# Performance work log

Hardware: AMD Instinct MI355X
Metric: run time of the kernel (lower is better)

Reference implementation:

```python
import jax, jax.numpy as jnp
import numpy as np
import math

DIM = 1536
HEAD_DIM = 128
N_HEADS = DIM // HEAD_DIM
B, S = 2, 2048
F, H, W = 8, 16, 16  # F*H*W == S
MAX_POS = 1024
EPS = 1e-6


def _make_freqs():
    # complex rotary freqs per Wan convention, split [22,21,21] over head_dim/2=64
    c = HEAD_DIM // 2
    sizes = [c - 2 * (c // 3), c // 3, c // 3]
    theta = 10000.0
    parts = []
    for s in sizes:
        inv = 1.0 / theta ** (np.arange(s, dtype=np.float64) / s)
        ang = np.arange(MAX_POS, dtype=np.float64)[:, None] * inv[None, :]
        parts.append(np.stack([np.cos(ang), np.sin(ang)], axis=-1))
    return jnp.asarray(np.concatenate(parts, axis=1), dtype=jnp.float32)  # [MAX_POS, 64, 2]


def setup_inputs() -> dict:
    key = jax.random.key(0)
    ks = jax.random.split(key, 12)
    std = 1.0 / math.sqrt(DIM)
    inp = {
        "x": jax.random.normal(ks[0], (B, S, DIM), jnp.float32),
        "seq_lens": jnp.full((B,), S, jnp.int32),
        "grid_sizes": jnp.tile(jnp.array([[F, H, W]], jnp.int32), (B, 1)),
        "freqs": _make_freqs(),
        "Wq": jax.random.normal(ks[1], (DIM, DIM), jnp.float32) * std,
        "bq": jnp.zeros((DIM,), jnp.float32),
        "Wk": jax.random.normal(ks[2], (DIM, DIM), jnp.float32) * std,
        "bk": jnp.zeros((DIM,), jnp.float32),
        "Wv": jax.random.normal(ks[3], (DIM, DIM), jnp.float32) * std,
        "bv": jnp.zeros((DIM,), jnp.float32),
        "Wo": jax.random.normal(ks[4], (DIM, DIM), jnp.float32) * std,
        "bo": jnp.zeros((DIM,), jnp.float32),
        "wq_norm": jnp.ones((DIM,), jnp.float32),
        "wk_norm": jnp.ones((DIM,), jnp.float32),
    }
    return inp


def _rmsnorm(x, w):
    x32 = x.astype(jnp.float32)
    return x32 * jax.lax.rsqrt(jnp.mean(x32 * x32, axis=-1, keepdims=True) + EPS) * w


def _rope_apply(x, grid_sizes, freqs):
    # x: [B, S, N, D]; grid sizes uniform across batch -> vectorized (no per-sample loop)
    f, h, w = (int(v) for v in np.asarray(grid_sizes)[0])
    s_rot = f * h * w
    Bx, Sx, N, D = x.shape
    c = D // 2
    s0, s1 = c - 2 * (c // 3), c // 3
    cos, sin = freqs[..., 0], freqs[..., 1]

    def grid_cs(t):  # build [s_rot, c] table
        tf = jnp.broadcast_to(t[:f, None, None, :s0], (f, h, w, s0))
        th = jnp.broadcast_to(t[None, :h, None, s0:s0 + s1], (f, h, w, s1))
        tw = jnp.broadcast_to(t[None, None, :w, s0 + s1:s0 + 2 * s1], (f, h, w, s1))
        return jnp.concatenate([tf, th, tw], axis=-1).reshape(s_rot, 1, c)

    fc, fs = grid_cs(cos), grid_cs(sin)  # [s_rot, 1, c]
    xr = x[:, :s_rot].astype(jnp.float32).reshape(Bx, s_rot, N, c, 2)
    a, b = xr[..., 0], xr[..., 1]
    out = jnp.stack([a * fc - b * fs, a * fs + b * fc], axis=-1).reshape(Bx, s_rot, N, D)
    if s_rot < Sx:
        out = jnp.concatenate([out, x[:, s_rot:].astype(jnp.float32)], axis=1)
    return out


def reference(x, seq_lens, grid_sizes, freqs, Wq, bq, Wk, bk, Wv, bv, Wo, bo, wq_norm, wk_norm):
    Bx, Sx, dim = x.shape
    N, D = N_HEADS, HEAD_DIM
    q = _rmsnorm(x @ Wq.T + bq, wq_norm).reshape(Bx, Sx, N, D)
    k = _rmsnorm(x @ Wk.T + bk, wk_norm).reshape(Bx, Sx, N, D)
    v = (x @ Wv.T + bv).reshape(Bx, Sx, N, D)
    q = _rope_apply(q, grid_sizes, freqs)
    k = _rope_apply(k, grid_sizes, freqs)
    scores = jnp.einsum("bsnd,btnd->bnst", q, k) / math.sqrt(D)  # [B,N,S,S]
    kmask = jnp.arange(Sx)[None, :] < seq_lens[:, None]          # [B,S] over keys
    scores = jnp.where(kmask[:, None, None, :], scores, -1e30)
    attn = jax.nn.softmax(scores, axis=-1)
    out = jnp.einsum("bnst,btnd->bsnd", attn, v).reshape(Bx, Sx, dim)
    return out @ Wo.T + bo
```

## Files before the change

kernel.cpp:

```cpp
#include <hip/hip_runtime.h>

typedef __attribute__((ext_vector_type(8))) short bf16x8;
typedef __attribute__((ext_vector_type(8))) unsigned short ushort8;
typedef __attribute__((ext_vector_type(4))) float f32x4;
typedef __attribute__((ext_vector_type(16))) float f32x16;
typedef unsigned short u16;
typedef unsigned int u32;

__device__ inline float bf2f(u16 u) {
    unsigned int x = ((unsigned int)u) << 16;
    float f; __builtin_memcpy(&f, &x, 4); return f;
}
__device__ inline u16 f2bf(float f) {
    unsigned int x; __builtin_memcpy(&x, &f, 4);
    unsigned int r = (x + 0x7FFFu + ((x >> 16) & 1u)) >> 16;
    return (u16)r;
}
__device__ inline u32 cvtpk(float lo, float hi) {
    u32 r;
    asm("v_cvt_pk_bf16_f32 %0, %1, %2" : "=v"(r) : "v"(lo), "v"(hi));
    return r;
}
__device__ inline void store_out(u16* p, float v) { *p = f2bf(v); }
__device__ inline void store_out(float* p, float v) { *p = v; }

__global__ __launch_bounds__(256) void f32_to_bf16_kernel(const float* __restrict__ src,
                                                          u16* __restrict__ dst, int n8) {
    int i = blockIdx.x * 256 + threadIdx.x;
    if (i >= n8) return;
    float4 a = *(const float4*)(src + (size_t)i * 8);
    float4 b = *(const float4*)(src + (size_t)i * 8 + 4);
    ushort8 o;
    o[0] = f2bf(a.x); o[1] = f2bf(a.y); o[2] = f2bf(a.z); o[3] = f2bf(a.w);
    o[4] = f2bf(b.x); o[5] = f2bf(b.y); o[6] = f2bf(b.z); o[7] = f2bf(b.w);
    *(ushort8*)(dst + (size_t)i * 8) = o;
}

__global__ __launch_bounds__(256) void prep2_kernel(const float* __restrict__ Wq, const float* __restrict__ Wk,
                                                    const float* __restrict__ Wv, const float* __restrict__ Wo,
                                                    const float* __restrict__ bq, const float* __restrict__ bk,
                                                    const float* __restrict__ bv, const float* __restrict__ freqs,
                                                    u16* __restrict__ wqkv, u16* __restrict__ wob,
                                                    float* __restrict__ bqkv, float* __restrict__ rope) {
    int bid = blockIdx.x, t = threadIdx.x;
    if (bid < 4608) {
        int i = bid * 256 + t;
        int seg = i / 294912, j = i - seg * 294912;
        const float* src = (seg == 0) ? Wq : (seg == 1) ? Wk : (seg == 2) ? Wv : Wo;
        u16* dst = (seg < 3) ? (wqkv + (size_t)seg * 2359296) : wob;
        float4 a = *(const float4*)(src + (size_t)j * 8);
        float4 b = *(const float4*)(src + (size_t)j * 8 + 4);
        ushort8 o;
        o[0] = f2bf(a.x); o[1] = f2bf(a.y); o[2] = f2bf(a.z); o[3] = f2bf(a.w);
        o[4] = f2bf(b.x); o[5] = f2bf(b.y); o[6] = f2bf(b.z); o[7] = f2bf(b.w);
        *(ushort8*)(dst + (size_t)j * 8) = o;
    } else if (bid < 5120) {
        int i = (bid - 4608) * 256 + t;
        int s = i >> 6, j = i & 63;
        int fi = s >> 8, hi = (s >> 4) & 15, wi = s & 15;
        int pos = (j < 22) ? fi : ((j < 43) ? hi : wi);
        rope[s * 128 + j * 2]     = freqs[pos * 128 + j * 2];
        rope[s * 128 + j * 2 + 1] = freqs[pos * 128 + j * 2 + 1];
    } else {
#pragma unroll
        for (int it = 0; it < 18; ++it) {
            int j = it * 256 + t;
            bqkv[j] = (j < 1536) ? bq[j] : ((j < 3072) ? bk[j - 1536] : bv[j - 3072]);
        }
    }
}

template <typename OutT>
__global__ __launch_bounds__(256) void gemm_bt(const u16* __restrict__ A, const u16* __restrict__ Bw,
                                               const float* __restrict__ bias, OutT* __restrict__ C,
                                               int M, int N, int K) {
    __shared__ __align__(16) u16 As[3][4096];
    __shared__ __align__(16) u16 Bs[3][4096];
    const int tid = threadIdx.x;
    const int w = tid >> 6, l = tid & 63;
    const int lg = l >> 4, li = l & 15;
    const int row0 = blockIdx.x * 128, col0 = blockIdx.y * 128;
    const int wr = (w >> 1) * 64, wc = (w & 1) * 64;
    const int nt = K >> 5;

    f32x4 acc[4][4] = {};

    auto STAGE = [&](int bi, int t) {
        int k0 = t << 5;
#pragma unroll
        for (int c = 0; c < 2; ++c) {
            int idx = c * 256 + tid;
            int r = idx >> 2;
            int clog = (idx & 3) ^ ((r >> 1) & 3);
            __builtin_amdgcn_global_load_lds(
                (const __attribute__((address_space(1))) void*)(A + (size_t)(row0 + r) * K + k0 + clog * 8),
                (__attribute__((address_space(3))) void*)((char*)&As[0][0] + bi * 8192 + c * 4096 + w * 1024), 16, 0, 0);
            __builtin_amdgcn_global_load_lds(
                (const __attribute__((address_space(1))) void*)(Bw + (size_t)(col0 + r) * K + k0 + clog * 8),
                (__attribute__((address_space(3))) void*)((char*)&Bs[0][0] + bi * 8192 + c * 4096 + w * 1024), 16, 0, 0);
        }
    };

    const int rchunk = (lg ^ ((li >> 1) & 3)) * 8;
    STAGE(0, 0);
    STAGE(1, 1);
    for (int tb = 0; tb < nt; tb += 3) {
#pragma unroll
        for (int j = 0; j < 3; ++j) {
            const int t = tb + j;
            if (t + 2 < nt) {
                STAGE((j + 2) % 3, t + 2);
                asm volatile("s_waitcnt vmcnt(8)" ::: "memory");
            } else if (t + 1 < nt) {
                asm volatile("s_waitcnt vmcnt(4)" ::: "memory");
            } else {
                asm volatile("s_waitcnt vmcnt(0)" ::: "memory");
            }
            __builtin_amdgcn_s_barrier();
            __builtin_amdgcn_sched_barrier(0);
            const u16* as = &As[j][0];
            const u16* bs = &Bs[j][0];
            bf16x8 af[4], bfr[4];
#pragma unroll
            for (int m = 0; m < 4; ++m) af[m] = *(const bf16x8*)(as + (wr + m * 16 + li) * 32 + rchunk);
#pragma unroll
            for (int n = 0; n < 4; ++n) bfr[n] = *(const bf16x8*)(bs + (wc + n * 16 + li) * 32 + rchunk);
#pragma unroll
            for (int m = 0; m < 4; ++m)
#pragma unroll
                for (int n = 0; n < 4; ++n)
                    acc[m][n] = __builtin_amdgcn_mfma_f32_16x16x32_bf16(af[m], bfr[n], acc[m][n], 0, 0, 0);
            __builtin_amdgcn_sched_barrier(0);
            __builtin_amdgcn_s_barrier();
        }
    }

#pragma unroll
    for (int m = 0; m < 4; ++m) {
#pragma unroll
        for (int n = 0; n < 4; ++n) {
#pragma unroll
            for (int j = 0; j < 4; ++j) {
                int r = row0 + wr + m * 16 + lg * 4 + j;
                int cc = col0 + wc + n * 16 + li;
                float v = acc[m][n][j] + bias[cc];
                store_out(&C[(size_t)r * N + cc], v);
            }
        }
    }
}

__global__ __launch_bounds__(256) void rmsview_kernel(const u16* __restrict__ qkv,
                                                      const float* __restrict__ wq_n,
                                                      const float* __restrict__ wk_n,
                                                      const float* __restrict__ rope,
                                                      u16* __restrict__ qh, u16* __restrict__ kh,
                                                      u16* __restrict__ vt) {
    __shared__ __align__(16) char sm[9216];
    int t = threadIdx.x;
    if (blockIdx.x < 4096) {
        int row = blockIdx.x;
        int b = row >> 11, s = row & 2047;
        const u16* pr = qkv + (size_t)row * 4608;
        int c0 = t * 6;

        float q[6], k[6];
#pragma unroll
        for (int i = 0; i < 3; ++i) {
            ushort2 uq = *(const ushort2*)(pr + c0 + 2 * i);
            ushort2 uk = *(const ushort2*)(pr + 1536 + c0 + 2 * i);
            q[2 * i] = bf2f(uq.x); q[2 * i + 1] = bf2f(uq.y);
            k[2 * i] = bf2f(uk.x); k[2 * i + 1] = bf2f(uk.y);
        }
        float sq = 0.f, sk = 0.f;
#pragma unroll
        for (int i = 0; i < 6; ++i) { sq += q[i] * q[i]; sk += k[i] * k[i]; }
#pragma unroll
        for (int off = 32; off >= 1; off >>= 1) {
            sq += __shfl_down(sq, off);
            sk += __shfl_down(sk, off);
        }
        float* red = (float*)sm;
        int w = t >> 6, l = t & 63;
        if (l == 0) { red[w] = sq; red[w + 4] = sk; }
        __syncthreads();
        float rq = rsqrtf((red[0] + red[1] + red[2] + red[3]) * (1.0f / 1536.0f) + 1e-6f);
        float rk = rsqrtf((red[4] + red[5] + red[6] + red[7]) * (1.0f / 1536.0f) + 1e-6f);

#pragma unroll
        for (int i = 0; i < 3; ++i) {
            int c = c0 + 2 * i;
            int h = c >> 7, d = c & 127;
            float cs = rope[s * 128 + d];
            float sn = rope[s * 128 + d + 1];
            float qa = q[2 * i] * rq * wq_n[c], qb = q[2 * i + 1] * rq * wq_n[c + 1];
            float ka = k[2 * i] * rk * wk_n[c], kb = k[2 * i + 1] * rk * wk_n[c + 1];
            size_t o = ((size_t)(b * 12 + h) * 2048 + s) * 128 + d;
            ushort2 qo, ko;
            qo.x = f2bf(qa * cs - qb * sn); qo.y = f2bf(qa * sn + qb * cs);
            ko.x = f2bf(ka * cs - kb * sn); ko.y = f2bf(ka * sn + kb * cs);
            *(ushort2*)(qh + o) = qo;
            *(ushort2*)(kh + o) = ko;
        }
    } else {
        int idx = blockIdx.x - 4096;
        const int s0 = (idx & 31) * 64;
        const int d0 = ((idx >> 5) & 1) * 64;
        const int bh = idx >> 6;
        const int b = bh / 12, h = bh % 12;
        u16* L = (u16*)sm;

#pragma unroll
        for (int j = 0; j < 2; ++j) {
            int p = j * 256 + t;
            int s = p >> 3, c8 = p & 7;
            ushort8 v8 = *(const ushort8*)(qkv + (size_t)(b * 2048 + s0 + s) * 4608 + 3072 + h * 128 + d0 + c8 * 8);
            int pb = c8 ^ ((s >> 3) & 7);
            *(ushort8*)(L + s * 72 + pb * 8) = v8;
        }
        __syncthreads();
#pragma unroll
        for (int j = 0; j < 2; ++j) {
            int p = j * 256 + t;
            int d = p >> 3, s8 = p & 7;
            ushort8 o;
#pragma unroll
            for (int i = 0; i < 8; ++i) {
                int ps = s8 * 8 + i;
                int v4 = ps & 15;
                int ls = (ps & ~15) | (v4 & 3) | ((v4 & 4) << 1) | ((v4 & 8) >> 1);
                o[i] = L[ls * 72 + ((((d >> 3) ^ (ls >> 3)) & 7) << 3) + (d & 7)];
            }
            *(ushort8*)(vt + (size_t)bh * 128 * 2048 + (size_t)(d0 + d) * 2048 + s0 + s8 * 8) = o;
        }
    }
}

__global__ __launch_bounds__(256, 2) void attn_kernel(const u16* __restrict__ qh, const u16* __restrict__ kh,
                                                      const u16* __restrict__ vt, const int* __restrict__ seq_lens,
                                                      u16* __restrict__ aout) {
    const int bid = blockIdx.x;
    const int g = bid & 7, rr = bid >> 3;
    const int bh = g * 3 + rr % 3;
    const int qt = rr / 3;
    const int b = bh / 12, h = bh % 12;
    const int tid = threadIdx.x;
    const int w = tid >> 6, l = tid & 63;
    const int q5 = l & 31;
    const int hi = l >> 5;
    const int seqlen = seq_lens[b];

    __shared__ __align__(16) char smem[65536];

    const size_t hbase = (size_t)bh * 2048 * 128;
    const u16* kb = kh + hbase;
    const u16* vtb = vt + hbase;

    const int qrow = qt * 128 + w * 32 + q5;
    bf16x8 qf[8];
    {
        const u16* qp = qh + hbase + (size_t)qrow * 128 + hi * 8;
#pragma unroll
        for (int kd = 0; kd < 8; ++kd) qf[kd] = *(const bf16x8*)(qp + kd * 16);
    }

    auto STAGE = [&](int bi, int kv0) {
#pragma unroll
        for (int i = 0; i < 4; ++i) {
            int p = i * 256 + tid;
            int kr = p >> 4, kc = p & 15;
            __builtin_amdgcn_global_load_lds(
                (const __attribute__((address_space(1))) void*)(kb + (size_t)(kv0 + kr) * 128 + ((kc ^ (kr & 15)) << 3)),
                (__attribute__((address_space(3))) void*)(smem + bi * 16384 + i * 4096 + w * 1024), 16, 0, 0);
            int vr = p >> 3, vc = p & 7;
            __builtin_amdgcn_global_load_lds(
                (const __attribute__((address_space(1))) void*)(vtb + (size_t)vr * 2048 + kv0 + ((vc ^ (vr & 7)) << 3)),
                (__attribute__((address_space(3))) void*)(smem + 32768 + bi * 16384 + i * 4096 + w * 1024), 16, 0, 0);
        }
    };

    f32x16 oacc[4] = {};
    float m_run = -3e38f, l_run = 0.f;
    const float c2 = 0.08838834764831845f * 1.44269504088896341f;

    STAGE(0, 0);
    for (int t = 0; t < 32; ++t) {
        const int cur = t & 1;
        const int kv0 = t * 64;
        if (t < 31) {
            STAGE(cur ^ 1, kv0 + 64);
            asm volatile("s_waitcnt vmcnt(8)" ::: "memory");
        } else {
            asm volatile("s_waitcnt vmcnt(0)" ::: "memory");
        }
        __builtin_amdgcn_s_barrier();
        __builtin_amdgcn_sched_barrier(0);

        const u16* Ks = (const u16*)(smem + cur * 16384);
        const u16* Vs = (const u16*)(smem + 32768 + cur * 16384);

        f32x16 sacc[2] = {};
        __builtin_amdgcn_s_setprio(1);
#pragma unroll
        for (int tt = 0; tt < 2; ++tt) {
            int row = tt * 32 + q5;
#pragma unroll
            for (int kd = 0; kd < 8; ++kd) {
                int bk = (2 * kd + hi) ^ (q5 & 15);
                bf16x8 kf = *(const bf16x8*)(Ks + row * 128 + bk * 8);
                sacc[tt] = __builtin_amdgcn_mfma_f32_32x32x16_bf16(kf, qf[kd], sacc[tt], 0, 0, 0);
            }
        }
        __builtin_amdgcn_s_setprio(0);

        if (kv0 + 64 > seqlen) {
#pragma unroll
            for (int tt = 0; tt < 2; ++tt)
#pragma unroll
                for (int m = 0; m < 4; ++m)
#pragma unroll
                    for (int r = 0; r < 4; ++r) {
                        int kv = kv0 + tt * 32 + m * 8 + hi * 4 + r;
                        if (kv >= seqlen) sacc[tt][m * 4 + r] = -1e30f;
                    }
        }

        float a8[8];
#pragma unroll
        for (int r = 0; r < 8; ++r)
            a8[r] = fmaxf(fmaxf(sacc[0][r], sacc[0][r + 8]), fmaxf(sacc[1][r], sacc[1][r + 8]));
        float b4_0 = fmaxf(a8[0], a8[1]), b4_1 = fmaxf(a8[2], a8[3]);
        float b4_2 = fmaxf(a8[4], a8[5]), b4_3 = fmaxf(a8[6], a8[7]);
        float pmax = fmaxf(fmaxf(b4_0, b4_1), fmaxf(b4_2, b4_3));
        pmax = fmaxf(pmax, __shfl_xor(pmax, 32));

        int defer = __all(pmax <= m_run + 62.7f);
        if (!defer) {
            float mnew = fmaxf(m_run, pmax);
            float alpha = __builtin_amdgcn_exp2f((m_run - mnew) * c2);
#pragma unroll
            for (int dt = 0; dt < 4; ++dt)
#pragma unroll
                for (int r = 0; r < 16; ++r) oacc[dt][r] *= alpha;
            l_run *= alpha;
            m_run = mnew;
        }

        float gs[8];
        u32 Wp[2][4][2];
#pragma unroll
        for (int tt = 0; tt < 2; ++tt)
#pragma unroll
            for (int m = 0; m < 4; ++m) {
                float p0 = __builtin_amdgcn_exp2f((sacc[tt][4 * m + 0] - m_run) * c2);
                float p1 = __builtin_amdgcn_exp2f((sacc[tt][4 * m + 1] - m_run) * c2);
                float p2 = __builtin_amdgcn_exp2f((sacc[tt][4 * m + 2] - m_run) * c2);
                float p3 = __builtin_amdgcn_exp2f((sacc[tt][4 * m + 3] - m_run) * c2);
                gs[tt * 4 + m] = (p0 + p1) + (p2 + p3);
                Wp[tt][m][0] = cvtpk(p0, p1);
                Wp[tt][m][1] = cvtpk(p2, p3);
            }
        float ls = ((gs[0] + gs[1]) + (gs[2] + gs[3])) + ((gs[4] + gs[5]) + (gs[6] + gs[7]));
        ls += __shfl_xor(ls, 32);
        l_run += ls;

        __builtin_amdgcn_s_setprio(1);
#pragma unroll
        for (int tt = 0; tt < 2; ++tt)
#pragma unroll
            for (int c = 0; c < 2; ++c) {
                union { u32 u[4]; bf16x8 v; } pu;
                pu.u[0] = Wp[tt][2 * c][0]; pu.u[1] = Wp[tt][2 * c][1];
                pu.u[2] = Wp[tt][2 * c + 1][0]; pu.u[3] = Wp[tt][2 * c + 1][1];
                int bk = 4 * tt + 2 * c + hi;
#pragma unroll
                for (int dt = 0; dt < 4; ++dt) {
                    int drow = dt * 32 + q5;
                    int pb = bk ^ (drow & 7);
                    bf16x8 vf = *(const bf16x8*)(Vs + drow * 64 + pb * 8);
                    oacc[dt] = __builtin_amdgcn_mfma_f32_32x32x16_bf16(vf, pu.v, oacc[dt], 0, 0, 0);
                }
            }
        __builtin_amdgcn_s_setprio(0);
        __builtin_amdgcn_sched_barrier(0);
        __builtin_amdgcn_s_barrier();
    }

    __syncthreads();
    u32* Lq = (u32*)smem + w * 2144;
    float inv_l = 1.0f / l_run;
#pragma unroll
    for (int dt = 0; dt < 4; ++dt)
#pragma unroll
        for (int m = 0; m < 4; ++m) {
            u32 w0 = cvtpk(oacc[dt][4 * m + 0] * inv_l, oacc[dt][4 * m + 1] * inv_l);
            u32 w1 = cvtpk(oacc[dt][4 * m + 2] * inv_l, oacc[dt][4 * m + 3] * inv_l);
            int widx = dt * 16 + 4 * m + 2 * hi;
            Lq[q5 * 67 + widx] = w0;
            Lq[q5 * 67 + widx + 1] = w1;
        }
    __builtin_amdgcn_s_waitcnt(0);
#pragma unroll
    for (int pp = 0; pp < 8; ++pp) {
        int qq = pp * 4 + (l >> 4);
        int cc = l & 15;
        union { u32 u[4]; ushort8 v; } ou;
        ou.u[0] = Lq[qq * 67 + cc * 4 + 0];
        ou.u[1] = Lq[qq * 67 + cc * 4 + 1];
        ou.u[2] = Lq[qq * 67 + cc * 4 + 2];
        ou.u[3] = Lq[qq * 67 + cc * 4 + 3];
        size_t off = ((size_t)(b * 2048 + qt * 128 + w * 32 + qq)) * 1536 + h * 128 + cc * 8;
        *(ushort8*)(aout + off) = ou.v;
    }
}

extern "C" void kernel_launch(void* const* d_in, const int* in_sizes, int n_in,
                              void* d_out, int out_size, void* d_ws, size_t ws_size,
                              hipStream_t stream) {
    const float* x    = (const float*)d_in[0];
    const int* seqlen = (const int*)d_in[1];
    const float* freqs = (const float*)d_in[3];
    const float* Wq = (const float*)d_in[4];  const float* bq = (const float*)d_in[5];
    const float* Wk = (const float*)d_in[6];  const float* bk = (const float*)d_in[7];
    const float* Wv = (const float*)d_in[8];  const float* bv = (const float*)d_in[9];
    const float* Wo = (const float*)d_in[10]; const float* bo = (const float*)d_in[11];
    const float* wqn = (const float*)d_in[12];
    const float* wkn = (const float*)d_in[13];
    float* out = (float*)d_out;

    char* ws = (char*)d_ws;
    u16*   xb   = (u16*)(ws);
    u16*   wqkv = (u16*)(ws + 12582912);
    u16*   wob  = (u16*)(ws + 26738688);
    float* bqkv = (float*)(ws + 31457280);
    float* rope = (float*)(ws + 31475712);
    u16*   qkv  = (u16*)(ws + 32524288);
    u16*   qhb  = (u16*)(ws + 70273024);
    u16*   khb  = (u16*)(ws + 82855936);
    u16*   vtb  = (u16*)(ws + 95438848);
    u16*   aob  = (u16*)(ws + 108021760);

    f32_to_bf16_kernel<<<3072, 256, 0, stream>>>(x, xb, 786432);
    prep2_kernel<<<5121, 256, 0, stream>>>(Wq, Wk, Wv, Wo, bq, bk, bv, freqs, wqkv, wob, bqkv, rope);

    gemm_bt<u16><<<dim3(32, 36), 256, 0, stream>>>(xb, wqkv, bqkv, qkv, 4096, 4608, 1536);
    rmsview_kernel<<<5632, 256, 0, stream>>>(qkv, wqn, wkn, rope, qhb, khb, vtb);
    attn_kernel<<<384, 256, 0, stream>>>(qhb, khb, vtb, seqlen, aob);
    gemm_bt<float><<<dim3(32, 12), 256, 0, stream>>>(aob, wob, bo, out, 4096, 1536, 1536);
}
```

Baseline: 218.1 us.

## Widen QKV GEMM tile to 128x256 and merge x conversion into prep kernel

Adds a gemm_wide kernel in which each block computes a 128x256 output tile, so each wave holds a 64x128 accumulator and A tiles are reused across twice as many columns. This halves the QKV projection grid to 32x18 blocks and cuts redundant A loads. It also folds the x fp32-to-bf16 conversion into the weight prep kernel, saving one launch. The cost is more registers and LDS per block (launch bounds of 2 blocks per SM), and 576 blocks may fill the CUs less evenly.

```diff
diff --git a/kernel.cpp b/kernel.cpp
--- a/kernel.cpp
+++ b/kernel.cpp
@@ -24,38 +24,35 @@
 __device__ inline void store_out(u16* p, float v) { *p = f2bf(v); }
 __device__ inline void store_out(float* p, float v) { *p = v; }
 
-__global__ __launch_bounds__(256) void f32_to_bf16_kernel(const float* __restrict__ src,
-                                                          u16* __restrict__ dst, int n8) {
-    int i = blockIdx.x * 256 + threadIdx.x;
-    if (i >= n8) return;
-    float4 a = *(const float4*)(src + (size_t)i * 8);
-    float4 b = *(const float4*)(src + (size_t)i * 8 + 4);
-    ushort8 o;
-    o[0] = f2bf(a.x); o[1] = f2bf(a.y); o[2] = f2bf(a.z); o[3] = f2bf(a.w);
-    o[4] = f2bf(b.x); o[5] = f2bf(b.y); o[6] = f2bf(b.z); o[7] = f2bf(b.w);
-    *(ushort8*)(dst + (size_t)i * 8) = o;
-}
-
-__global__ __launch_bounds__(256) void prep2_kernel(const float* __restrict__ Wq, const float* __restrict__ Wk,
-                                                    const float* __restrict__ Wv, const float* __restrict__ Wo,
-                                                    const float* __restrict__ bq, const float* __restrict__ bk,
-                                                    const float* __restrict__ bv, const float* __restrict__ freqs,
-                                                    u16* __restrict__ wqkv, u16* __restrict__ wob,
-                                                    float* __restrict__ bqkv, float* __restrict__ rope) {
+__global__ __launch_bounds__(256) void prep_kernel(const float* __restrict__ x,
+                                                   const float* __restrict__ Wq, const float* __restrict__ Wk,
+                                                   const float* __restrict__ Wv, const float* __restrict__ Wo,
+                                                   const float* __restrict__ bq, const float* __restrict__ bk,
+                                                   const float* __restrict__ bv, const float* __restrict__ freqs,
+                                                   u16* __restrict__ xb,
+                                                   u16* __restrict__ wqkv, u16* __restrict__ wob,
+                                                   float* __restrict__ bqkv, float* __restrict__ rope) {
     int bid = blockIdx.x, t = threadIdx.x;
-    if (bid < 4608) {
-        int i = bid * 256 + t;
-        int seg = i / 294912, j = i - seg * 294912;
-        const float* src = (seg == 0) ? Wq : (seg == 1) ? Wk : (seg == 2) ? Wv : Wo;
-        u16* dst = (seg < 3) ? (wqkv + (size_t)seg * 2359296) : wob;
-        float4 a = *(const float4*)(src + (size_t)j * 8);
-        float4 b = *(const float4*)(src + (size_t)j * 8 + 4);
+    if (bid < 7680) {
+        const float* src;
+        u16* dst;
+        size_t j;
+        if (bid < 3072) {
+            src = x; dst = xb; j = (size_t)bid * 256 + t;
+        } else {
+            size_t i = (size_t)(bid - 3072) * 256 + t;
+            int seg = (int)(i / 294912); j = i - (size_t)seg * 294912;
+            src = (seg == 0) ? Wq : (seg == 1) ? Wk : (seg == 2) ? Wv : Wo;
+            dst = (seg < 3) ? (wqkv + (size_t)seg * 2359296) : wob;
+        }
+        float4 a = *(const float4*)(src + j * 8);
+        float4 b = *(const float4*)(src + j * 8 + 4);
         ushort8 o;
         o[0] = f2bf(a.x); o[1] = f2bf(a.y); o[2] = f2bf(a.z); o[3] = f2bf(a.w);
         o[4] = f2bf(b.x); o[5] = f2bf(b.y); o[6] = f2bf(b.z); o[7] = f2bf(b.w);
-        *(ushort8*)(dst + (size_t)j * 8) = o;
-    } else if (bid < 5120) {
-        int i = (bid - 4608) * 256 + t;
+        *(ushort8*)(dst + j * 8) = o;
+    } else if (bid < 8192) {
+        int i = (bid - 7680) * 256 + t;
         int s = i >> 6, j = i & 63;
         int fi = s >> 8, hi = (s >> 4) & 15, wi = s & 15;
         int pos = (j < 22) ? fi : ((j < 43) ? hi : wi);
@@ -66,6 +63,92 @@
         for (int it = 0; it < 18; ++it) {
             int j = it * 256 + t;
             bqkv[j] = (j < 1536) ? bq[j] : ((j < 3072) ? bk[j - 1536] : bv[j - 3072]);
+        }
+    }
+}
+
+template <typename OutT>
+__global__ __launch_bounds__(256, 2) void gemm_wide(const u16* __restrict__ A, const u16* __restrict__ Bw,
+                                                    const float* __restrict__ bias, OutT* __restrict__ C,
+                                                    int M, int N, int K) {
+    __shared__ __align__(16) u16 As[3][4096];
+    __shared__ __align__(16) u16 Bs[3][8192];
+    const int tid = threadIdx.x;
+    const int w = tid >> 6, l = tid & 63;
+    const int lg = l >> 4, li = l & 15;
+    const int row0 = blockIdx.x * 128, col0 = blockIdx.y * 256;
+    const int wr = (w >> 1) * 64, wc = (w & 1) * 128;
+    const int nt = K >> 5;
+
+    f32x4 acc[4][8] = {};
+
+    auto STAGE = [&](int bi, int t) {
+        int k0 = t << 5;
+#pragma unroll
+        for (int c = 0; c < 2; ++c) {
+            int idx = c * 256 + tid;
+            int r = idx >> 2;
+            int clog = (idx & 3) ^ ((r >> 1) & 3);
+            __builtin_amdgcn_global_load_lds(
+                (const __attribute__((address_space(1))) void*)(A + (size_t)(row0 + r) * K + k0 + clog * 8),
+                (__attribute__((address_space(3))) void*)((char*)&As[0][0] + bi * 8192 + c * 4096 + w * 1024), 16, 0, 0);
+        }
+#pragma unroll
+        for (int c = 0; c < 4; ++c) {
+            int idx = c * 256 + tid;
+            int r = idx >> 2;
+            int clog = (idx & 3) ^ ((r >> 1) & 3);
+            __builtin_amdgcn_global_load_lds(
+                (const __attribute__((address_space(1))) void*)(Bw + (size_t)(col0 + r) * K + k0 + clog * 8),
+                (__attribute__((address_space(3))) void*)((char*)&Bs[0][0] + bi * 16384 + c * 4096 + w * 1024), 16, 0, 0);
+        }
+    };
+
+    const int rchunk = (lg ^ ((li >> 1) & 3)) * 8;
+    STAGE(0, 0);
+    STAGE(1, 1);
+    for (int tb = 0; tb < nt; tb += 3) {
+#pragma unroll
+        for (int j = 0; j < 3; ++j) {
+            const int t = tb + j;
+            if (t + 2 < nt) {
+                STAGE((j + 2) % 3, t + 2);
+                asm volatile("s_waitcnt vmcnt(12)" ::: "memory");
+            } else if (t + 1 < nt) {
+                asm volatile("s_waitcnt vmcnt(6)" ::: "memory");
+            } else {
+                asm volatile("s_waitcnt vmcnt(0)" ::: "memory");
+            }
+            __builtin_amdgcn_s_barrier();
+            __builtin_amdgcn_sched_barrier(0);
+            const u16* as = &As[j][0];
+            const u16* bs = &Bs[j][0];
+            bf16x8 af[4], bfr[8];
+#pragma unroll
+            for (int m = 0; m < 4; ++m) af[m] = *(const bf16x8*)(as + (wr + m * 16 + li) * 32 + rchunk);
+#pragma unroll
+            for (int n = 0; n < 8; ++n) bfr[n] = *(const bf16x8*)(bs + (wc + n * 16 + li) * 32 + rchunk);
+#pragma unroll
+            for (int m = 0; m < 4; ++m)
+#pragma unroll
+                for (int n = 0; n < 8; ++n)
+                    acc[m][n] = __builtin_amdgcn_mfma_f32_16x16x32_bf16(af[m], bfr[n], acc[m][n], 0, 0, 0);
+            __builtin_amdgcn_sched_barrier(0);
+            __builtin_amdgcn_s_barrier();
+        }
+    }
+
+#pragma unroll
+    for (int m = 0; m < 4; ++m) {
+#pragma unroll
+        for (int n = 0; n < 8; ++n) {
+#pragma unroll
+            for (int j = 0; j < 4; ++j) {
+                int r = row0 + wr + m * 16 + lg * 4 + j;
+                int cc = col0 + wc + n * 16 + li;
+                float v = acc[m][n][j] + bias[cc];
+                store_out(&C[(size_t)r * N + cc], v);
+            }
         }
     }
 }
@@ -440,10 +523,9 @@
     u16*   vtb  = (u16*)(ws + 95438848);
     u16*   aob  = (u16*)(ws + 108021760);
 
-    f32_to_bf16_kernel<<<3072, 256, 0, stream>>>(x, xb, 786432);
-    prep2_kernel<<<5121, 256, 0, stream>>>(Wq, Wk, Wv, Wo, bq, bk, bv, freqs, wqkv, wob, bqkv, rope);
-
-    gemm_bt<u16><<<dim3(32, 36), 256, 0, stream>>>(xb, wqkv, bqkv, qkv, 4096, 4608, 1536);
+    prep_kernel<<<8193, 256, 0, stream>>>(x, Wq, Wk, Wv, Wo, bq, bk, bv, freqs, xb, wqkv, wob, bqkv, rope);
+
+    gemm_wide<u16><<<dim3(32, 18), 256, 0, stream>>>(xb, wqkv, bqkv, qkv, 4096, 4608, 1536);
     rmsview_kernel<<<5632, 256, 0, stream>>>(qkv, wqn, wkn, rope, qhb, khb, vtb);
     attn_kernel<<<384, 256, 0, stream>>>(qhb, khb, vtb, seqlen, aob);
     gemm_bt<float><<<dim3(32, 12), 256, 0, stream>>>(aob, wob, bo, out, 4096, 1536, 1536);
```

New measurement: 233.1 us. 6.9% more time.

## Load GEMM A operand directly into registers and merge prep kernels

Applied to the files above, without the earlier changes.

The GEMM kernel no longer stages the A tile through LDS. Each wave loads its A fragments straight from global memory into registers, double-buffered one k-step ahead, while B keeps the three-stage LDS pipeline; the wait counts and the unroll factor of 6 are adjusted to match. Separately, the x-to-bf16 conversion is folded into the weight/rope prep kernel to save one launch. The aim is to cut LDS traffic and barrier pressure for A, at the cost of less coalesced global loads with exposed latency and more registers per thread.

```diff
diff --git a/kernel.cpp b/kernel.cpp
--- a/kernel.cpp
+++ b/kernel.cpp
@@ -24,38 +24,35 @@
 __device__ inline void store_out(u16* p, float v) { *p = f2bf(v); }
 __device__ inline void store_out(float* p, float v) { *p = v; }
 
-__global__ __launch_bounds__(256) void f32_to_bf16_kernel(const float* __restrict__ src,
-                                                          u16* __restrict__ dst, int n8) {
-    int i = blockIdx.x * 256 + threadIdx.x;
-    if (i >= n8) return;
-    float4 a = *(const float4*)(src + (size_t)i * 8);
-    float4 b = *(const float4*)(src + (size_t)i * 8 + 4);
-    ushort8 o;
-    o[0] = f2bf(a.x); o[1] = f2bf(a.y); o[2] = f2bf(a.z); o[3] = f2bf(a.w);
-    o[4] = f2bf(b.x); o[5] = f2bf(b.y); o[6] = f2bf(b.z); o[7] = f2bf(b.w);
-    *(ushort8*)(dst + (size_t)i * 8) = o;
-}
-
-__global__ __launch_bounds__(256) void prep2_kernel(const float* __restrict__ Wq, const float* __restrict__ Wk,
-                                                    const float* __restrict__ Wv, const float* __restrict__ Wo,
-                                                    const float* __restrict__ bq, const float* __restrict__ bk,
-                                                    const float* __restrict__ bv, const float* __restrict__ freqs,
-                                                    u16* __restrict__ wqkv, u16* __restrict__ wob,
-                                                    float* __restrict__ bqkv, float* __restrict__ rope) {
+__global__ __launch_bounds__(256) void prep_kernel(const float* __restrict__ x,
+                                                   const float* __restrict__ Wq, const float* __restrict__ Wk,
+                                                   const float* __restrict__ Wv, const float* __restrict__ Wo,
+                                                   const float* __restrict__ bq, const float* __restrict__ bk,
+                                                   const float* __restrict__ bv, const float* __restrict__ freqs,
+                                                   u16* __restrict__ xb,
+                                                   u16* __restrict__ wqkv, u16* __restrict__ wob,
+                                                   float* __restrict__ bqkv, float* __restrict__ rope) {
     int bid = blockIdx.x, t = threadIdx.x;
-    if (bid < 4608) {
-        int i = bid * 256 + t;
-        int seg = i / 294912, j = i - seg * 294912;
-        const float* src = (seg == 0) ? Wq : (seg == 1) ? Wk : (seg == 2) ? Wv : Wo;
-        u16* dst = (seg < 3) ? (wqkv + (size_t)seg * 2359296) : wob;
-        float4 a = *(const float4*)(src + (size_t)j * 8);
-        float4 b = *(const float4*)(src + (size_t)j * 8 + 4);
+    if (bid < 7680) {
+        const float* src;
+        u16* dst;
+        size_t j;
+        if (bid < 3072) {
+            src = x; dst = xb; j = (size_t)bid * 256 + t;
+        } else {
+            size_t i = (size_t)(bid - 3072) * 256 + t;
+            int seg = (int)(i / 294912); j = i - (size_t)seg * 294912;
+            src = (seg == 0) ? Wq : (seg == 1) ? Wk : (seg == 2) ? Wv : Wo;
+            dst = (seg < 3) ? (wqkv + (size_t)seg * 2359296) : wob;
+        }
+        float4 a = *(const float4*)(src + j * 8);
+        float4 b = *(const float4*)(src + j * 8 + 4);
         ushort8 o;
         o[0] = f2bf(a.x); o[1] = f2bf(a.y); o[2] = f2bf(a.z); o[3] = f2bf(a.w);
         o[4] = f2bf(b.x); o[5] = f2bf(b.y); o[6] = f2bf(b.z); o[7] = f2bf(b.w);
-        *(ushort8*)(dst + (size_t)j * 8) = o;
-    } else if (bid < 5120) {
-        int i = (bid - 4608) * 256 + t;
+        *(ushort8*)(dst + j * 8) = o;
+    } else if (bid < 8192) {
+        int i = (bid - 7680) * 256 + t;
         int s = i >> 6, j = i & 63;
         int fi = s >> 8, hi = (s >> 4) & 15, wi = s & 15;
         int pos = (j < 22) ? fi : ((j < 43) ? hi : wi);
@@ -71,10 +68,9 @@
 }
 
 template <typename OutT>
-__global__ __launch_bounds__(256) void gemm_bt(const u16* __restrict__ A, const u16* __restrict__ Bw,
-                                               const float* __restrict__ bias, OutT* __restrict__ C,
-                                               int M, int N, int K) {
-    __shared__ __align__(16) u16 As[3][4096];
+__global__ __launch_bounds__(256) void gemm_areg(const u16* __restrict__ A, const u16* __restrict__ Bw,
+                                                 const float* __restrict__ bias, OutT* __restrict__ C,
+                                                 int M, int N, int K) {
     __shared__ __align__(16) u16 Bs[3][4096];
     const int tid = threadIdx.x;
     const int w = tid >> 6, l = tid & 63;
@@ -93,24 +89,34 @@
             int r = idx >> 2;
             int clog = (idx & 3) ^ ((r >> 1) & 3);
             __builtin_amdgcn_global_load_lds(
-                (const __attribute__((address_space(1))) void*)(A + (size_t)(row0 + r) * K + k0 + clog * 8),
-                (__attribute__((address_space(3))) void*)((char*)&As[0][0] + bi * 8192 + c * 4096 + w * 1024), 16, 0, 0);
-            __builtin_amdgcn_global_load_lds(
                 (const __attribute__((address_space(1))) void*)(Bw + (size_t)(col0 + r) * K + k0 + clog * 8),
                 (__attribute__((address_space(3))) void*)((char*)&Bs[0][0] + bi * 8192 + c * 4096 + w * 1024), 16, 0, 0);
         }
     };
 
-    const int rchunk = (lg ^ ((li >> 1) & 3)) * 8;
+    const u16* ap[4];
+#pragma unroll
+    for (int m = 0; m < 4; ++m) ap[m] = A + (size_t)(row0 + wr + m * 16 + li) * K + lg * 8;
+
+    bf16x8 af2[2][4];
+#pragma unroll
+    for (int m = 0; m < 4; ++m) af2[0][m] = *(const bf16x8*)(ap[m]);
     STAGE(0, 0);
     STAGE(1, 1);
-    for (int tb = 0; tb < nt; tb += 3) {
-#pragma unroll
-        for (int j = 0; j < 3; ++j) {
+
+    const int rchunk = (lg ^ ((li >> 1) & 3)) * 8;
+    for (int tb = 0; tb < nt; tb += 6) {
+#pragma unroll
+        for (int j = 0; j < 6; ++j) {
             const int t = tb + j;
+            if (t + 1 < nt) {
+#pragma unroll
+                for (int m = 0; m < 4; ++m)
+                    af2[(j + 1) & 1][m] = *(const bf16x8*)(ap[m] + (size_t)(t + 1) * 32);
+            }
             if (t + 2 < nt) {
                 STAGE((j + 2) % 3, t + 2);
-                asm volatile("s_waitcnt vmcnt(8)" ::: "memory");
+                asm volatile("s_waitcnt vmcnt(6)" ::: "memory");
             } else if (t + 1 < nt) {
                 asm volatile("s_waitcnt vmcnt(4)" ::: "memory");
             } else {
@@ -118,18 +124,15 @@
             }
             __builtin_amdgcn_s_barrier();
             __builtin_amdgcn_sched_barrier(0);
-            const u16* as = &As[j][0];
-            const u16* bs = &Bs[j][0];
-            bf16x8 af[4], bfr[4];
-#pragma unroll
-            for (int m = 0; m < 4; ++m) af[m] = *(const bf16x8*)(as + (wr + m * 16 + li) * 32 + rchunk);
+            const u16* bs = &Bs[j % 3][0];
+            bf16x8 bfr[4];
 #pragma unroll
             for (int n = 0; n < 4; ++n) bfr[n] = *(const bf16x8*)(bs + (wc + n * 16 + li) * 32 + rchunk);
 #pragma unroll
             for (int m = 0; m < 4; ++m)
 #pragma unroll
                 for (int n = 0; n < 4; ++n)
-                    acc[m][n] = __builtin_amdgcn_mfma_f32_16x16x32_bf16(af[m], bfr[n], acc[m][n], 0, 0, 0);
+                    acc[m][n] = __builtin_amdgcn_mfma_f32_16x16x32_bf16(af2[j & 1][m], bfr[n], acc[m][n], 0, 0, 0);
             __builtin_amdgcn_sched_barrier(0);
             __builtin_amdgcn_s_barrier();
         }
@@ -440,11 +443,10 @@
     u16*   vtb  = (u16*)(ws + 95438848);
     u16*   aob  = (u16*)(ws + 108021760);
 
-    f32_to_bf16_kernel<<<3072, 256, 0, stream>>>(x, xb, 786432);
-    prep2_kernel<<<5121, 256, 0, stream>>>(Wq, Wk, Wv, Wo, bq, bk, bv, freqs, wqkv, wob, bqkv, rope);
-
-    gemm_bt<u16><<<dim3(32, 36), 256, 0, stream>>>(xb, wqkv, bqkv, qkv, 4096, 4608, 1536);
+    prep_kernel<<<8193, 256, 0, stream>>>(x, Wq, Wk, Wv, Wo, bq, bk, bv, freqs, xb, wqkv, wob, bqkv, rope);
+
+    gemm_areg<u16><<<dim3(32, 36), 256, 0, stream>>>(xb, wqkv, bqkv, qkv, 4096, 4608, 1536);
     rmsview_kernel<<<5632, 256, 0, stream>>>(qkv, wqn, wkn, rope, qhb, khb, vtb);
     attn_kernel<<<384, 256, 0, stream>>>(qhb, khb, vtb, seqlen, aob);
-    gemm_bt<float><<<dim3(32, 12), 256, 0, stream>>>(aob, wob, bo, out, 4096, 1536, 1536);
-}
+    gemm_areg<float><<<dim3(32, 12), 256, 0, stream>>>(aob, wob, bo, out, 4096, 1536, 1536);
+}
```

Measured after the change: 300.4 us, median of 2. 37.7% more time.
